# Kernel tuning notes

Measured on AMD Instinct MI355X. Metric: run time of the kernel, lower is better.

Reference implementation:

```python
import jax, jax.numpy as jnp
import numpy as np

T, D, DFF, E, K = 2048, 1024, 2816, 8, 2


def setup_inputs() -> dict:
    key = jax.random.key(0)
    k1, k2, k3, k4, k5, k6 = jax.random.split(key, 6)
    return {
        "x": jax.random.normal(k1, (T, D), dtype=jnp.float32),
        "topk_weight": jax.random.uniform(k2, (T, K), dtype=jnp.float32),
        "gate_w": jax.random.normal(k3, (E, DFF, D), dtype=jnp.float32) * 0.02,
        "up_w": jax.random.normal(k4, (E, DFF, D), dtype=jnp.float32) * 0.02,
        "down_w": jax.random.normal(k5, (E, D, DFF), dtype=jnp.float32) * 0.02,
        "topk_ids": jax.random.randint(k6, (T, K), 0, E, dtype=jnp.int64),
    }


def reference(x, topk_weight, gate_w, up_w, down_w, topk_ids):
    # x: [T, D]; topk_ids/topk_weight: [T, K]
    # Per expert: SwiGLU MLP over all tokens, combined with the per-token
    # routing weight for that expert (0 if the expert was not selected).
    out = jnp.zeros_like(x)
    num_experts = gate_w.shape[0]
    for e in range(num_experts):
        h = jax.nn.silu(x @ gate_w[e].T) * (x @ up_w[e].T)  # [T, DFF]
        y = h @ down_w[e].T                                  # [T, D]
        # sum over top-k slots of routing weight where this expert was chosen
        w_e = jnp.sum(jnp.where(topk_ids == e, topk_weight, 0.0), axis=1)  # [T]
        out = out + y * w_e[:, None]
    return out
```

## Files before the change

### kernel.cpp

```cpp
#include <hip/hip_runtime.h>
#include <stdint.h>

typedef __attribute__((ext_vector_type(8))) __bf16 bf16x8;
typedef __attribute__((ext_vector_type(4))) float f32x4;
typedef __attribute__((ext_vector_type(8))) unsigned short ushort8;

#define T_TOK 2048
#define D_DIM 1024
#define DFF   2816
#define NEXP  8
#define NROWS 4096
#define BK    32
#define NW_ELEM (NEXP * DFF * D_DIM)
#define MAXTM2 24

#define SWZ(r,g) ((g) ^ (((r) >> 1) & 3))

#define TL_N    0
#define TL_BASE 16
#define TL_VAL  80
#define TL_EXP  144

__device__ __forceinline__ void lds_cp16(const void* g, void* l) {
  __builtin_amdgcn_global_load_lds(
      (const __attribute__((address_space(1))) void*)g,
      (__attribute__((address_space(3))) void*)l, 16, 0, 0);
}

__device__ __forceinline__ ushort8 pack_bf16x8(float4 a, float4 b) {
  union { __bf16 h[8]; ushort8 u; } r;
  r.h[0] = (__bf16)a.x; r.h[1] = (__bf16)a.y; r.h[2] = (__bf16)a.z; r.h[3] = (__bf16)a.w;
  r.h[4] = (__bf16)b.x; r.h[5] = (__bf16)b.y; r.h[6] = (__bf16)b.z; r.h[7] = (__bf16)b.w;
  return r.u;
}

__device__ __forceinline__ unsigned short f2bf(float f) {
  union { __bf16 h; unsigned short u; } r;
  r.h = (__bf16)f;
  return r.u;
}

__device__ __forceinline__ float bf2f(unsigned short u) {
  union { uint32_t u; float f; } v; v.u = (uint32_t)u << 16;
  return v.f;
}

__device__ __forceinline__ int xcd_chunk(int bid, int nwork) {
  const int q = nwork >> 3, r = nwork & 7;
  const int xcd = bid & 7;
  const int base = (xcd < r) ? xcd * (q + 1) : r * (q + 1) + (xcd - r) * q;
  return base + (bid >> 3);
}

__global__ __launch_bounds__(512) void routing_kernel(
    const int* __restrict__ ids, const float* __restrict__ w,
    int* __restrict__ cnt, int* __restrict__ off,
    int* __restrict__ tok, float* __restrict__ wgt, int* __restrict__ rowmap,
    int* __restrict__ tl2)
{
  __shared__ int s_cnt[NEXP];
  __shared__ int s_off[NEXP];
  const int lane = threadIdx.x & 63;
  const int e    = threadIdx.x >> 6;

  int total = 0;
  for (int c = 0; c < NROWS / 64; ++c) {
    int id = ids[c * 64 + lane];
    unsigned long long b = __ballot(id == e);
    total += __popcll(b);
  }
  if (lane == 0) s_cnt[e] = total;
  __syncthreads();
  if (threadIdx.x == 0) {
    int acc = 0, n2 = 0;
    for (int i = 0; i < NEXP; ++i) {
      s_off[i] = acc; off[i] = acc; cnt[i] = s_cnt[i];
      for (int j = 0; j < s_cnt[i]; j += 256) {
        tl2[TL_BASE + n2] = acc + j;
        tl2[TL_VAL  + n2] = min(256, s_cnt[i] - j);
        tl2[TL_EXP  + n2] = i;
        ++n2;
      }
      acc += s_cnt[i];
    }
    tl2[TL_N] = n2;
  }
  __syncthreads();
  int base = s_off[e];
  for (int c = 0; c < NROWS / 64; ++c) {
    int idx = c * 64 + lane;
    int id = ids[idx];
    bool m = (id == e);
    unsigned long long b = __ballot(m);
    int pos = __popcll(b & ((1ull << lane) - 1ull));
    if (m) {
      tok[base + pos] = idx >> 1;
      wgt[base + pos] = w[idx];
      rowmap[idx] = base + pos;
    }
    base += __popcll(b);
  }
}

__global__ __launch_bounds__(256) void gather_x_kernel(
    const float* __restrict__ x, const int* __restrict__ tok,
    unsigned short* __restrict__ xg)
{
  const int i = blockIdx.x;
  const int t = tok[i];
  const float4 v = ((const float4*)(x + (size_t)t * D_DIM))[threadIdx.x];
  ushort4 o;
  o.x = f2bf(v.x); o.y = f2bf(v.y); o.z = f2bf(v.z); o.w = f2bf(v.w);
  ((ushort4*)(xg + (size_t)i * D_DIM))[threadIdx.x] = o;
}

#define BM_A 256
#define BN_A 64
#define NT_A (DFF / BN_A)
#define NWORK_A (MAXTM2 * NT_A)
#define WCD_BLKS 1024
#define NWG_A (NWORK_A + WCD_BLKS)
#define KT_A (D_DIM / BK)

__global__ __launch_bounds__(512) void moe_gateup_f32r(
    const float* __restrict__ gate_w, const float* __restrict__ up_w,
    const unsigned short* __restrict__ xg, const float* __restrict__ wgt,
    const int* __restrict__ tl2,
    unsigned short* __restrict__ hbuf,
    const float* __restrict__ down_w, unsigned short* __restrict__ dbuf)
{
  const int bid = blockIdx.x;
  const int ntm = tl2[TL_N];
  const int nwork = ntm * NT_A;
  const int tid = threadIdx.x;
  if (bid >= nwork) {
    if (bid >= NWORK_A) {
      const int c = bid - NWORK_A;
      const size_t stride = (size_t)WCD_BLKS * 512;
      for (size_t i = (size_t)c * 512 + tid; i < NW_ELEM / 8; i += stride) {
        const size_t idx = i * 8;
        float4 a = *(const float4*)(down_w + idx);
        float4 b = *(const float4*)(down_w + idx + 4);
        *(ushort8*)(dbuf + idx) = pack_bf16x8(a, b);
      }
    }
    return;
  }
  const int w = xcd_chunk(bid, nwork);
  const int tile = w / NT_A;
  const int nt   = w % NT_A;
  const int row_base = tl2[TL_BASE + tile];
  const int valid    = tl2[TL_VAL  + tile];
  const int e        = tl2[TL_EXP  + tile];
  const int n0 = nt * BN_A;

  __shared__ __align__(16) unsigned short Alds[3][BM_A * BK];
  __shared__ __align__(16) unsigned short Bg[3][BN_A * BK];
  __shared__ __align__(16) unsigned short Bu[3][BN_A * BK];

  const int lane = tid & 63;
  const int wid = tid >> 6;
  const int wm = wid >> 1, wn = wid & 1;
  const int lhi = lane >> 4, llo = lane & 15;

  f32x4 accg[4][2], accu[4][2];
  #pragma unroll
  for (int i = 0; i < 4; ++i)
    #pragma unroll
    for (int j = 0; j < 2; ++j) {
      accg[i][j] = (f32x4){0.f, 0.f, 0.f, 0.f};
      accu[i][j] = (f32x4){0.f, 0.f, 0.f, 0.f};
    }

  const int ar0 = tid >> 2, ag = tid & 3;
  const int ar1 = ar0 + 128;
  const size_t a_src0 = (size_t)(row_base + min(ar0, valid - 1)) * D_DIM + SWZ(ar0, ag) * 8;
  const size_t a_src1 = (size_t)(row_base + min(ar1, valid - 1)) * D_DIM + SWZ(ar1, ag) * 8;

  const int q2 = tid & 255;
  const int br = q2 >> 2, bg2 = q2 & 3;
  const float* bsrc = ((tid < 256) ? gate_w : up_w)
                    + ((size_t)e * DFF + n0 + br) * D_DIM + bg2 * 8;
  const int bws = br * BK + SWZ(br, bg2) * 8;
  unsigned short* bdst[3];
  bdst[0] = (tid < 256) ? &Bg[0][bws] : &Bu[0][bws];
  bdst[1] = (tid < 256) ? &Bg[1][bws] : &Bu[1][bws];
  bdst[2] = (tid < 256) ? &Bg[2][bws] : &Bu[2][bws];

  {
    float4 c0 = *(const float4*)(bsrc);
    float4 c1 = *(const float4*)(bsrc + 4);
    *(ushort8*)bdst[0] = pack_bf16x8(c0, c1);
  }
  float4 pb0 = *(const float4*)(bsrc + BK);
  float4 pb1 = *(const float4*)(bsrc + BK + 4);
  lds_cp16(xg + a_src0, &Alds[0][tid * 8]);
  lds_cp16(xg + a_src1, &Alds[0][(tid + 512) * 8]);
  lds_cp16(xg + a_src0 + BK, &Alds[1][tid * 8]);
  lds_cp16(xg + a_src1 + BK, &Alds[1][(tid + 512) * 8]);
  asm volatile("s_waitcnt vmcnt(0) lgkmcnt(0)" ::: "memory");
  __builtin_amdgcn_s_barrier();

  int cur = 0;
  for (int t = 0; t < KT_A; ++t) {
    const int nxt = (cur + 1 >= 3) ? cur - 2 : cur + 1;
    const int nb  = (cur + 2 >= 3) ? cur - 1 : cur + 2;
    const int kn2 = (t + 2 < KT_A) ? (t + 2) * BK : 0;

    float4 nb0 = *(const float4*)(bsrc + kn2);
    float4 nb1 = *(const float4*)(bsrc + kn2 + 4);

    asm volatile("s_waitcnt vmcnt(6) lgkmcnt(0)" ::: "memory");
    __builtin_amdgcn_s_barrier();

    lds_cp16(xg + a_src0 + kn2, &Alds[nb][tid * 8]);
    lds_cp16(xg + a_src1 + kn2, &Alds[nb][(tid + 512) * 8]);
    *(ushort8*)bdst[nxt] = pack_bf16x8(pb0, pb1);

    bf16x8 a[4], bgf[2], buf_[2];
    #pragma unroll
    for (int mi = 0; mi < 4; ++mi) {
      int row = wm * 64 + mi * 16 + llo;
      a[mi] = *(const bf16x8*)&Alds[cur][row * BK + SWZ(row, lhi) * 8];
    }
    #pragma unroll
    for (int ni = 0; ni < 2; ++ni) {
      int row = wn * 32 + ni * 16 + llo;
      bgf[ni]  = *(const bf16x8*)&Bg[cur][row * BK + SWZ(row, lhi) * 8];
      buf_[ni] = *(const bf16x8*)&Bu[cur][row * BK + SWZ(row, lhi) * 8];
    }
    __builtin_amdgcn_s_setprio(1);
    #pragma unroll
    for (int mi = 0; mi < 4; ++mi)
      #pragma unroll
      for (int ni = 0; ni < 2; ++ni) {
        accg[mi][ni] = __builtin_amdgcn_mfma_f32_16x16x32_bf16(a[mi], bgf[ni], accg[mi][ni], 0, 0, 0);
        accu[mi][ni] = __builtin_amdgcn_mfma_f32_16x16x32_bf16(a[mi], buf_[ni], accu[mi][ni], 0, 0, 0);
      }
    __builtin_amdgcn_s_setprio(0);

    pb0 = nb0; pb1 = nb1;
    cur = (cur + 1 >= 3) ? 0 : cur + 1;
  }

  #pragma unroll
  for (int mi = 0; mi < 4; ++mi) {
    #pragma unroll
    for (int r = 0; r < 4; ++r) {
      int row = wm * 64 + mi * 16 + lhi * 4 + r;
      if (row < valid) {
        int grow = row_base + row;
        float wv = wgt[grow];
        size_t base = (size_t)grow * DFF + n0 + wn * 32;
        #pragma unroll
        for (int ni = 0; ni < 2; ++ni) {
          float g = accg[mi][ni][r];
          float u = accu[mi][ni][r];
          float h = (g / (1.f + __expf(-g))) * u * wv;
          hbuf[base + ni * 16 + llo] = f2bf(h);
        }
      }
    }
  }
}

#define BM_B 256
#define BN_B 128
#define NT_B (D_DIM / BN_B)
#define SLICES_B 4
#define NWT_B (NT_B * SLICES_B)
#define NWG_B (MAXTM2 * NWT_B)

#define PIPE_BARRIER_VM3() do { \
    asm volatile("s_waitcnt vmcnt(3)" ::: "memory"); \
    __builtin_amdgcn_s_barrier(); \
  } while (0)

template <bool USE_YBUF>
__global__ __launch_bounds__(512) void moe_down_bf(
    const unsigned short* __restrict__ dbuf,
    const unsigned short* __restrict__ hbuf,
    const int* __restrict__ tok,
    const int* __restrict__ tl2,
    unsigned short* __restrict__ ybuf, float* __restrict__ out_atomic)
{
  constexpr int KS = DFF / SLICES_B;
  constexpr int KT = KS / BK;

  const int bid = blockIdx.x;
  const int ntm = tl2[TL_N];
  const int nwork = ntm * NWT_B;
  if (bid >= nwork) return;
  const int w = xcd_chunk(bid, nwork);
  const int tile = w / NWT_B;
  const int rr   = w % NWT_B;
  const int nt = rr & 7;
  const int sl = rr >> 3;
  const int row_base = tl2[TL_BASE + tile];
  const int valid    = tl2[TL_VAL  + tile];
  const int e        = tl2[TL_EXP  + tile];
  const int n0 = nt * BN_B;
  const int kbeg = sl * KS;

  __shared__ __align__(16) unsigned short Alds[3][BM_B * BK];
  __shared__ __align__(16) unsigned short Blds[3][BN_B * BK];

  const int tid = threadIdx.x, lane = tid & 63, wid = tid >> 6;
  const int wm = wid >> 1, wn = wid & 1;
  const int lhi = lane >> 4, llo = lane & 15;

  f32x4 acc[4][4];
  #pragma unroll
  for (int i = 0; i < 4; ++i)
    #pragma unroll
    for (int j = 0; j < 4; ++j) acc[i][j] = (f32x4){0.f, 0.f, 0.f, 0.f};

  const unsigned short* db = dbuf + ((size_t)e * D_DIM + n0) * DFF;

  const int ar0 = tid >> 2, ag = tid & 3;
  const int ar1 = ar0 + 128;
  const size_t a_src0 = (size_t)(row_base + min(ar0, valid - 1)) * DFF + SWZ(ar0, ag) * 8;
  const size_t a_src1 = (size_t)(row_base + min(ar1, valid - 1)) * DFF + SWZ(ar1, ag) * 8;
  const int brr = tid >> 2, bgg = tid & 3;
  const size_t b_src = (size_t)brr * DFF + SWZ(brr, bgg) * 8;

  lds_cp16(hbuf + a_src0 + kbeg, &Alds[0][tid * 8]);
  lds_cp16(hbuf + a_src1 + kbeg, &Alds[0][(tid + 512) * 8]);
  lds_cp16(db + b_src + kbeg, &Blds[0][tid * 8]);
  {
    const int k1 = kbeg + BK;
    lds_cp16(hbuf + a_src0 + k1, &Alds[1][tid * 8]);
    lds_cp16(hbuf + a_src1 + k1, &Alds[1][(tid + 512) * 8]);
    lds_cp16(db + b_src + k1, &Blds[1][tid * 8]);
  }

  int cur = 0;
  for (int t = 0; t < KT; ++t) {
    PIPE_BARRIER_VM3();

    const int nb = (cur + 2 >= 3) ? cur - 1 : cur + 2;
    const int kn = kbeg + ((t + 2 < KT) ? (t + 2) * BK : 0);
    lds_cp16(hbuf + a_src0 + kn, &Alds[nb][tid * 8]);
    lds_cp16(hbuf + a_src1 + kn, &Alds[nb][(tid + 512) * 8]);
    lds_cp16(db + b_src + kn, &Blds[nb][tid * 8]);

    bf16x8 a[4], b[4];
    #pragma unroll
    for (int mi = 0; mi < 4; ++mi) {
      int row = wm * 64 + mi * 16 + llo;
      a[mi] = *(const bf16x8*)&Alds[cur][row * BK + SWZ(row, lhi) * 8];
    }
    #pragma unroll
    for (int ni = 0; ni < 4; ++ni) {
      int row = wn * 64 + ni * 16 + llo;
      b[ni] = *(const bf16x8*)&Blds[cur][row * BK + SWZ(row, lhi) * 8];
    }
    __builtin_amdgcn_s_setprio(1);
    #pragma unroll
    for (int mi = 0; mi < 4; ++mi)
      #pragma unroll
      for (int ni = 0; ni < 4; ++ni)
        acc[mi][ni] = __builtin_amdgcn_mfma_f32_16x16x32_bf16(a[mi], b[ni], acc[mi][ni], 0, 0, 0);
    __builtin_amdgcn_s_setprio(0);

    cur = (cur + 1 >= 3) ? 0 : cur + 1;
  }

  #pragma unroll
  for (int mi = 0; mi < 4; ++mi) {
    #pragma unroll
    for (int r = 0; r < 4; ++r) {
      int row = wm * 64 + mi * 16 + lhi * 4 + r;
      if (row < valid) {
        if (USE_YBUF) {
          unsigned short* yp = ybuf + ((size_t)sl * NROWS + row_base + row) * D_DIM + n0 + wn * 64;
          #pragma unroll
          for (int ni = 0; ni < 4; ++ni) yp[ni * 16 + llo] = f2bf(acc[mi][ni][r]);
        } else {
          int tk = tok[row_base + row];
          float* op = out_atomic + (size_t)tk * D_DIM + n0 + wn * 64;
          #pragma unroll
          for (int ni = 0; ni < 4; ++ni) atomicAdd(op + ni * 16 + llo, acc[mi][ni][r]);
        }
      }
    }
  }
}

__global__ __launch_bounds__(256) void combine_kernel(
    const unsigned short* __restrict__ ybuf, const int* __restrict__ rowmap,
    float* __restrict__ out)
{
  const int t = blockIdx.x;
  const int d = threadIdx.x * 4;
  const int r0 = rowmap[t * 2], r1 = rowmap[t * 2 + 1];
  float s0 = 0.f, s1 = 0.f, s2 = 0.f, s3 = 0.f;
  #pragma unroll
  for (int sl = 0; sl < SLICES_B; ++sl) {
    ushort4 a = *(const ushort4*)(ybuf + ((size_t)sl * NROWS + r0) * D_DIM + d);
    ushort4 b = *(const ushort4*)(ybuf + ((size_t)sl * NROWS + r1) * D_DIM + d);
    s0 += bf2f(a.x) + bf2f(b.x);
    s1 += bf2f(a.y) + bf2f(b.y);
    s2 += bf2f(a.z) + bf2f(b.z);
    s3 += bf2f(a.w) + bf2f(b.w);
  }
  float4 s = {s0, s1, s2, s3};
  *(float4*)(out + (size_t)t * D_DIM + d) = s;
}

extern "C" void kernel_launch(void* const* d_in, const int* in_sizes, int n_in,
                              void* d_out, int out_size, void* d_ws, size_t ws_size,
                              hipStream_t stream) {
  const float* x      = (const float*)d_in[0];
  const float* topk_w = (const float*)d_in[1];
  const float* gate_w = (const float*)d_in[2];
  const float* up_w   = (const float*)d_in[3];
  const float* down_w = (const float*)d_in[4];
  const int*   ids    = (const int*)d_in[5];
  float* out = (float*)d_out;

  char* ws = (char*)d_ws;
  int*   cnt    = (int*)(ws + 0);
  int*   off    = (int*)(ws + 32);
  int*   tok    = (int*)(ws + 64);
  float* wgt    = (float*)(ws + 64 + NROWS * 4);
  int*   rowmap = (int*)(ws + 64 + NROWS * 8);
  int*   tl2    = (int*)(ws + 50688);

  const size_t XG_OFF = 65536;
  const size_t XG_SZ  = (size_t)NROWS * D_DIM * 2;
  const size_t HB_OFF = XG_OFF + XG_SZ;
  const size_t HB_SZ  = (size_t)NROWS * DFF * 2;
  const size_t W_SZ   = (size_t)NW_ELEM * 2;
  const size_t DB_OFF = HB_OFF + HB_SZ;
  const size_t YB_OFF = DB_OFF + W_SZ;
  const size_t YB_SZ  = (size_t)SLICES_B * NROWS * D_DIM * 2;

  unsigned short* xg   = (unsigned short*)(ws + XG_OFF);
  unsigned short* hbuf = (unsigned short*)(ws + HB_OFF);
  unsigned short* dbuf = (unsigned short*)(ws + DB_OFF);
  unsigned short* ybuf = (unsigned short*)(ws + YB_OFF);

  routing_kernel<<<1, 512, 0, stream>>>(ids, topk_w, cnt, off, tok, wgt, rowmap, tl2);
  gather_x_kernel<<<NROWS, 256, 0, stream>>>(x, tok, xg);
  moe_gateup_f32r<<<NWG_A, 512, 0, stream>>>(gate_w, up_w, xg, wgt, tl2, hbuf, down_w, dbuf);

  if (ws_size >= YB_OFF + YB_SZ) {
    moe_down_bf<true><<<NWG_B, 512, 0, stream>>>(dbuf, hbuf, tok, tl2, ybuf, nullptr);
    combine_kernel<<<T_TOK, 256, 0, stream>>>(ybuf, rowmap, out);
  } else {
    hipMemsetAsync(d_out, 0, (size_t)out_size * sizeof(float), stream);
    moe_down_bf<false><<<NWG_B, 512, 0, stream>>>(dbuf, hbuf, tok, tl2, nullptr, out);
  }
}
```

Measured before the change: 229.3 us.

## Convert down weights to bf16 inside down GEMM instead of a separate pass

Removes the extra blocks in the gate/up kernel that converted the whole f32 down_w tensor to a bf16 workspace buffer. The down GEMM now loads f32 weights through registers, packs them to bf16 and writes them to LDS, with register prefetch two stages ahead. This avoids writing and re-reading the bf16 copy. In exchange, every down tile reloads f32 weights (twice the bytes per tile, repeated across token tiles) through a register-staged path instead of direct global-to-LDS copies.

```diff
diff --git a/kernel.cpp b/kernel.cpp
--- a/kernel.cpp
+++ b/kernel.cpp
@@ -11,7 +11,6 @@
 #define NEXP  8
 #define NROWS 4096
 #define BK    32
-#define NW_ELEM (NEXP * DFF * D_DIM)
 #define MAXTM2 24
 
 #define SWZ(r,g) ((g) ^ (((r) >> 1) & 3))
@@ -117,35 +116,20 @@
 #define BM_A 256
 #define BN_A 64
 #define NT_A (DFF / BN_A)
-#define NWORK_A (MAXTM2 * NT_A)
-#define WCD_BLKS 1024
-#define NWG_A (NWORK_A + WCD_BLKS)
+#define NWG_A (MAXTM2 * NT_A)
 #define KT_A (D_DIM / BK)
 
 __global__ __launch_bounds__(512) void moe_gateup_f32r(
     const float* __restrict__ gate_w, const float* __restrict__ up_w,
     const unsigned short* __restrict__ xg, const float* __restrict__ wgt,
     const int* __restrict__ tl2,
-    unsigned short* __restrict__ hbuf,
-    const float* __restrict__ down_w, unsigned short* __restrict__ dbuf)
+    unsigned short* __restrict__ hbuf)
 {
   const int bid = blockIdx.x;
   const int ntm = tl2[TL_N];
   const int nwork = ntm * NT_A;
   const int tid = threadIdx.x;
-  if (bid >= nwork) {
-    if (bid >= NWORK_A) {
-      const int c = bid - NWORK_A;
-      const size_t stride = (size_t)WCD_BLKS * 512;
-      for (size_t i = (size_t)c * 512 + tid; i < NW_ELEM / 8; i += stride) {
-        const size_t idx = i * 8;
-        float4 a = *(const float4*)(down_w + idx);
-        float4 b = *(const float4*)(down_w + idx + 4);
-        *(ushort8*)(dbuf + idx) = pack_bf16x8(a, b);
-      }
-    }
-    return;
-  }
+  if (bid >= nwork) return;
   const int w = xcd_chunk(bid, nwork);
   const int tile = w / NT_A;
   const int nt   = w % NT_A;
@@ -271,14 +255,9 @@
 #define NWT_B (NT_B * SLICES_B)
 #define NWG_B (MAXTM2 * NWT_B)
 
-#define PIPE_BARRIER_VM3() do { \
-    asm volatile("s_waitcnt vmcnt(3)" ::: "memory"); \
-    __builtin_amdgcn_s_barrier(); \
-  } while (0)
-
 template <bool USE_YBUF>
-__global__ __launch_bounds__(512) void moe_down_bf(
-    const unsigned short* __restrict__ dbuf,
+__global__ __launch_bounds__(512) void moe_down_f32r(
+    const float* __restrict__ down_w,
     const unsigned short* __restrict__ hbuf,
     const int* __restrict__ tok,
     const int* __restrict__ tl2,
@@ -315,34 +294,44 @@
     #pragma unroll
     for (int j = 0; j < 4; ++j) acc[i][j] = (f32x4){0.f, 0.f, 0.f, 0.f};
 
-  const unsigned short* db = dbuf + ((size_t)e * D_DIM + n0) * DFF;
-
   const int ar0 = tid >> 2, ag = tid & 3;
   const int ar1 = ar0 + 128;
   const size_t a_src0 = (size_t)(row_base + min(ar0, valid - 1)) * DFF + SWZ(ar0, ag) * 8;
   const size_t a_src1 = (size_t)(row_base + min(ar1, valid - 1)) * DFF + SWZ(ar1, ag) * 8;
+
   const int brr = tid >> 2, bgg = tid & 3;
-  const size_t b_src = (size_t)brr * DFF + SWZ(brr, bgg) * 8;
-
+  const float* bsrc = down_w + ((size_t)e * D_DIM + n0 + brr) * DFF + bgg * 8 + kbeg;
+  const int bws = brr * BK + SWZ(brr, bgg) * 8;
+
+  {
+    float4 c0 = *(const float4*)(bsrc);
+    float4 c1 = *(const float4*)(bsrc + 4);
+    *(ushort8*)&Blds[0][bws] = pack_bf16x8(c0, c1);
+  }
+  float4 pb0 = *(const float4*)(bsrc + BK);
+  float4 pb1 = *(const float4*)(bsrc + BK + 4);
   lds_cp16(hbuf + a_src0 + kbeg, &Alds[0][tid * 8]);
   lds_cp16(hbuf + a_src1 + kbeg, &Alds[0][(tid + 512) * 8]);
-  lds_cp16(db + b_src + kbeg, &Blds[0][tid * 8]);
-  {
-    const int k1 = kbeg + BK;
-    lds_cp16(hbuf + a_src0 + k1, &Alds[1][tid * 8]);
-    lds_cp16(hbuf + a_src1 + k1, &Alds[1][(tid + 512) * 8]);
-    lds_cp16(db + b_src + k1, &Blds[1][tid * 8]);
-  }
+  lds_cp16(hbuf + a_src0 + kbeg + BK, &Alds[1][tid * 8]);
+  lds_cp16(hbuf + a_src1 + kbeg + BK, &Alds[1][(tid + 512) * 8]);
+  asm volatile("s_waitcnt vmcnt(0) lgkmcnt(0)" ::: "memory");
+  __builtin_amdgcn_s_barrier();
 
   int cur = 0;
   for (int t = 0; t < KT; ++t) {
-    PIPE_BARRIER_VM3();
-
-    const int nb = (cur + 2 >= 3) ? cur - 1 : cur + 2;
-    const int kn = kbeg + ((t + 2 < KT) ? (t + 2) * BK : 0);
-    lds_cp16(hbuf + a_src0 + kn, &Alds[nb][tid * 8]);
-    lds_cp16(hbuf + a_src1 + kn, &Alds[nb][(tid + 512) * 8]);
-    lds_cp16(db + b_src + kn, &Blds[nb][tid * 8]);
+    const int nxt = (cur + 1 >= 3) ? cur - 2 : cur + 1;
+    const int nb  = (cur + 2 >= 3) ? cur - 1 : cur + 2;
+    const int kn2 = (t + 2 < KT) ? (t + 2) * BK : 0;
+
+    float4 nb0 = *(const float4*)(bsrc + kn2);
+    float4 nb1 = *(const float4*)(bsrc + kn2 + 4);
+
+    asm volatile("s_waitcnt vmcnt(6) lgkmcnt(0)" ::: "memory");
+    __builtin_amdgcn_s_barrier();
+
+    lds_cp16(hbuf + a_src0 + kbeg + kn2, &Alds[nb][tid * 8]);
+    lds_cp16(hbuf + a_src1 + kbeg + kn2, &Alds[nb][(tid + 512) * 8]);
+    *(ushort8*)&Blds[nxt][bws] = pack_bf16x8(pb0, pb1);
 
     bf16x8 a[4], b[4];
     #pragma unroll
@@ -363,6 +352,7 @@
         acc[mi][ni] = __builtin_amdgcn_mfma_f32_16x16x32_bf16(a[mi], b[ni], acc[mi][ni], 0, 0, 0);
     __builtin_amdgcn_s_setprio(0);
 
+    pb0 = nb0; pb1 = nb1;
     cur = (cur + 1 >= 3) ? 0 : cur + 1;
   }
 
@@ -431,25 +421,22 @@
   const size_t XG_SZ  = (size_t)NROWS * D_DIM * 2;
   const size_t HB_OFF = XG_OFF + XG_SZ;
   const size_t HB_SZ  = (size_t)NROWS * DFF * 2;
-  const size_t W_SZ   = (size_t)NW_ELEM * 2;
-  const size_t DB_OFF = HB_OFF + HB_SZ;
-  const size_t YB_OFF = DB_OFF + W_SZ;
+  const size_t YB_OFF = HB_OFF + HB_SZ;
   const size_t YB_SZ  = (size_t)SLICES_B * NROWS * D_DIM * 2;
 
   unsigned short* xg   = (unsigned short*)(ws + XG_OFF);
   unsigned short* hbuf = (unsigned short*)(ws + HB_OFF);
-  unsigned short* dbuf = (unsigned short*)(ws + DB_OFF);
   unsigned short* ybuf = (unsigned short*)(ws + YB_OFF);
 
   routing_kernel<<<1, 512, 0, stream>>>(ids, topk_w, cnt, off, tok, wgt, rowmap, tl2);
   gather_x_kernel<<<NROWS, 256, 0, stream>>>(x, tok, xg);
-  moe_gateup_f32r<<<NWG_A, 512, 0, stream>>>(gate_w, up_w, xg, wgt, tl2, hbuf, down_w, dbuf);
+  moe_gateup_f32r<<<NWG_A, 512, 0, stream>>>(gate_w, up_w, xg, wgt, tl2, hbuf);
 
   if (ws_size >= YB_OFF + YB_SZ) {
-    moe_down_bf<true><<<NWG_B, 512, 0, stream>>>(dbuf, hbuf, tok, tl2, ybuf, nullptr);
+    moe_down_f32r<true><<<NWG_B, 512, 0, stream>>>(down_w, hbuf, tok, tl2, ybuf, nullptr);
     combine_kernel<<<T_TOK, 256, 0, stream>>>(ybuf, rowmap, out);
   } else {
     hipMemsetAsync(d_out, 0, (size_t)out_size * sizeof(float), stream);
-    moe_down_bf<false><<<NWG_B, 512, 0, stream>>>(dbuf, hbuf, tok, tl2, nullptr, out);
-  }
-}
+    moe_down_f32r<false><<<NWG_B, 512, 0, stream>>>(down_w, hbuf, tok, tl2, nullptr, out);
+  }
+}
```

Result: faster. 220.9 us (median of 2 runs) (-3.7%).
